# Kernel tuning notes

Hardware: AMD Instinct MI355X
Metric: run time of the kernel (lower is better)

## Reference

```python
import jax, jax.numpy as jnp
import numpy as np

N = 50000      # num nodes
E = 800000     # num edges
D = 128        # num_hid
EPS = 1e-8


def _mlp(x, w1, b1, w2, b2):
    # 2-layer MLP: Linear -> ReLU -> Linear (dropout disabled at inference)
    return jax.nn.relu(x @ w1 + b1) @ w2 + b2


def setup_inputs() -> dict:
    key = jax.random.key(0)
    ks = jax.random.split(key, 12)

    def lin(k, fan_in, fan_out):
        kw, kb = jax.random.split(k)
        lim = 1.0 / np.sqrt(fan_in)
        w = jax.random.uniform(kw, (fan_in, fan_out), jnp.float32, -lim, lim)
        b = jax.random.uniform(kb, (fan_out,), jnp.float32, -lim, lim)
        return w, b

    H = jax.random.normal(ks[0], (N, D), jnp.float32)
    edge_index = jax.random.randint(ks[1], (2, E), 0, N, jnp.int64)
    w1_1, b1_1 = lin(ks[2], 2 * D, D)   # mlp_1 layer 1
    w1_2, b1_2 = lin(ks[3], D, D)       # mlp_1 layer 2
    w2_1, b2_1 = lin(ks[4], 2 * D, D)   # mlp_2 layer 1
    w2_2, b2_2 = lin(ks[5], D, 1)       # mlp_2 layer 2 (channel_curv=False -> out=1)
    t = jnp.zeros((), jnp.float32)
    return {"t": t, "H": H, "edge_index": edge_index,
            "w1_1": w1_1, "b1_1": b1_1, "w1_2": w1_2, "b1_2": b1_2,
            "w2_1": w2_1, "b2_1": b2_1, "w2_2": w2_2, "b2_2": b2_2}


def reference(t, H, edge_index, w1_1, b1_1, w1_2, b1_2, w2_1, b2_1, w2_2, b2_2):
    src, dst = edge_index[0], edge_index[1]

    # damping: row-normalize H
    H = H / (jnp.linalg.norm(H, axis=1, keepdims=True) + EPS)

    H_i = H[src]                                    # [E, D]
    H_j = H[dst]                                    # [E, D]

    # curvature(H_i, H_j)
    c = jnp.concatenate((H_i, H_j), axis=1)         # [E, 2D]
    c = jax.nn.relu(_mlp(c, w1_1, b1_1, w1_2, b1_2))  # [E, D]
    c = jax.ops.segment_sum(c, src, num_segments=N)   # scatter-sum -> [N, D]
    c = jnp.concatenate((c[src], c[dst]), axis=1)     # [E, 2D]
    curv = _mlp(c, w2_1, b2_1, w2_2, b2_2)            # [E, 1]

    # damped edge message
    cos = jnp.sum(H_i * H_j, axis=1, keepdims=True)   # [E, 1]
    H_edge = curv * (H_j - cos * H_i)                 # [E, D]

    # scatter-mean over source node
    s = jax.ops.segment_sum(H_edge, src, num_segments=N)               # [N, D]
    cnt = jax.ops.segment_sum(jnp.ones((E, 1), H.dtype), src, num_segments=N)
    Hm = s / jnp.maximum(cnt, 1.0)

    # damping: row-normalize output
    return Hm / (jnp.linalg.norm(Hm, axis=1, keepdims=True) + EPS)
```

## Files before the change

### kernel.cpp

```cpp
#include <hip/hip_runtime.h>
#include <hip/hip_bf16.h>

#define D 128
#define EPS 1e-8f
#define E1S 136

typedef _Float16 f16;
typedef __attribute__((ext_vector_type(8))) _Float16 half8;
typedef __attribute__((ext_vector_type(4))) float f32x4;
typedef unsigned int uint;

__device__ inline float2 up2(uint u) {
    union { uint u; f16 h[2]; } v; v.u = u;
    return make_float2((float)v.h[0], (float)v.h[1]);
}

__global__ void k_normalize(const float* __restrict__ H, f16* __restrict__ Hn, int N) {
    int row = blockIdx.x * 4 + (threadIdx.x >> 6);
    int lane = threadIdx.x & 63;
    if (row >= N) return;
    float2 v = reinterpret_cast<const float2*>(H + (size_t)row * D)[lane];
    float ss = v.x * v.x + v.y * v.y;
    #pragma unroll
    for (int off = 32; off; off >>= 1) ss += __shfl_xor(ss, off, 64);
    float scale = 1.0f / (sqrtf(ss) + EPS);
    union { f16 h[2]; uint u; } p;
    p.h[0] = (f16)(v.x * scale);
    p.h[1] = (f16)(v.y * scale);
    reinterpret_cast<uint*>(Hn + (size_t)row * D)[lane] = p.u;
}

__global__ void k_hist(const int* __restrict__ src, int* __restrict__ deg, int E) {
    for (int e = blockIdx.x * blockDim.x + threadIdx.x; e < E; e += gridDim.x * blockDim.x)
        atomicAdd(&deg[src[e]], 1);
}

__global__ void k_scan(const int* __restrict__ deg, int* __restrict__ rowptr, int N) {
    __shared__ int wsum[16];
    __shared__ int carry;
    int t = threadIdx.x, lane = t & 63, w = t >> 6;
    if (t == 0) carry = 0;
    __syncthreads();
    for (int base = 0; base < N; base += 4096) {
        int i0 = base + t * 4;
        int a = 0, b = 0, c = 0, d = 0;
        if (i0 + 3 < N) {
            int4 v4 = *reinterpret_cast<const int4*>(deg + i0);
            a = v4.x; b = v4.y; c = v4.z; d = v4.w;
        } else {
            if (i0 < N) a = deg[i0];
            if (i0 + 1 < N) b = deg[i0 + 1];
            if (i0 + 2 < N) c = deg[i0 + 2];
            if (i0 + 3 < N) d = deg[i0 + 3];
        }
        int s1 = a + b, s2 = s1 + c, s3 = s2 + d;
        int v = s3;
        #pragma unroll
        for (int off = 1; off < 64; off <<= 1) {
            int u = __shfl_up(v, off, 64);
            if (lane >= off) v += u;
        }
        if (lane == 63) wsum[w] = v;
        __syncthreads();
        if (w == 0 && lane < 16) {
            int s = wsum[lane];
            #pragma unroll
            for (int off = 1; off < 16; off <<= 1) {
                int u = __shfl_up(s, off, 64);
                if (lane >= off) s += u;
            }
            wsum[lane] = s;
        }
        __syncthreads();
        int add = (w > 0 ? wsum[w - 1] : 0) + carry;
        int incl = v + add;
        int pre = incl - s3;
        if (i0 < N)     rowptr[i0 + 1] = pre + a;
        if (i0 + 1 < N) rowptr[i0 + 2] = pre + s1;
        if (i0 + 2 < N) rowptr[i0 + 3] = pre + s2;
        if (i0 + 3 < N) rowptr[i0 + 4] = pre + s3;
        __syncthreads();
        if (t == 1023) carry = incl;
        __syncthreads();
    }
    if (t == 0) rowptr[0] = 0;
}

__global__ void k_scatter(const int* __restrict__ src, const int* __restrict__ dst,
                          const int* __restrict__ rowptr, int* __restrict__ fill,
                          int* __restrict__ srcS, int* __restrict__ dstS, int E) {
    for (int e = blockIdx.x * blockDim.x + threadIdx.x; e < E; e += gridDim.x * blockDim.x) {
        int s = src[e];
        int pos = atomicAdd(&fill[s], 1);
        int idx = rowptr[s] + pos;
        srcS[idx] = s;
        dstS[idx] = dst[e];
    }
}

__global__ void k_prep_all(const float* __restrict__ w1_1, const float* __restrict__ w1_2,
                           const float* __restrict__ w2_1, f16* __restrict__ Wt) {
    int b = blockIdx.x;
    int m = b >> 6;
    int idx = (b & 63) * 256 + threadIdx.x;
    int k = idx >> 7, n = idx & 127;
    const float* W = (m == 0) ? w1_1
                   : (m == 1) ? w1_1 + 16384
                   : (m == 2) ? w1_2
                   : (m == 3) ? w2_1
                              : w2_1 + 16384;
    Wt[m * 16384 + n * 128 + k] = (f16)W[k * 128 + n];
}

template <bool A_F16>
__global__ __launch_bounds__(256, 4)
void k_gemm_dual(const void* __restrict__ Aptr, const f16* __restrict__ Wt0,
                 const f16* __restrict__ Wt1, const float* __restrict__ bias0,
                 f16* __restrict__ out0, f16* __restrict__ out1, int N) {
    __shared__ f16 As[64 * E1S];
    int t = threadIdx.x;
    int r0 = blockIdx.x * 64;
    int l = t & 63, w = t >> 6, n0 = w * 32;
    {
        int er = t >> 2, kb = (t & 3) * 32;
        int rc = min(r0 + er, N - 1);
        if (A_F16) {
            const half8* Ap = reinterpret_cast<const half8*>((const f16*)Aptr + (size_t)rc * 128 + kb);
            #pragma unroll
            for (int q = 0; q < 4; ++q)
                *reinterpret_cast<half8*>(&As[er * E1S + kb + q * 8]) = Ap[q];
        } else {
            const float4* Ap = reinterpret_cast<const float4*>((const float*)Aptr + (size_t)rc * 128 + kb);
            #pragma unroll
            for (int q = 0; q < 4; ++q) {
                float4 a0 = Ap[q * 2], a1 = Ap[q * 2 + 1];
                half8 sv;
                sv[0] = (f16)a0.x; sv[1] = (f16)a0.y; sv[2] = (f16)a0.z; sv[3] = (f16)a0.w;
                sv[4] = (f16)a1.x; sv[5] = (f16)a1.y; sv[6] = (f16)a1.z; sv[7] = (f16)a1.w;
                *reinterpret_cast<half8*>(&As[er * E1S + kb + q * 8]) = sv;
            }
        }
    }
    half8 bfrag[2][4];
    #pragma unroll
    for (int nt = 0; nt < 2; ++nt) {
        int col = n0 + nt * 16 + (l & 15);
        #pragma unroll
        for (int kt = 0; kt < 4; ++kt)
            bfrag[nt][kt] = *reinterpret_cast<const half8*>(Wt0 + col * 128 + kt * 32 + (l >> 4) * 8);
    }
    float b0a = bias0[n0 + (l & 15)];
    float b0b = bias0[n0 + 16 + (l & 15)];
    __syncthreads();
    f32x4 acc0[4][2], acc1[4][2];
    #pragma unroll
    for (int mt = 0; mt < 4; ++mt) {
        acc0[mt][0] = (f32x4){0,0,0,0}; acc0[mt][1] = (f32x4){0,0,0,0};
        acc1[mt][0] = (f32x4){0,0,0,0}; acc1[mt][1] = (f32x4){0,0,0,0};
    }
    #pragma unroll
    for (int mt = 0; mt < 4; ++mt) {
        int arow = mt * 16 + (l & 15);
        #pragma unroll
        for (int kt = 0; kt < 4; ++kt) {
            half8 af = *reinterpret_cast<const half8*>(&As[arow * E1S + kt * 32 + (l >> 4) * 8]);
            acc0[mt][0] = __builtin_amdgcn_mfma_f32_16x16x32_f16(af, bfrag[0][kt], acc0[mt][0], 0, 0, 0);
            acc0[mt][1] = __builtin_amdgcn_mfma_f32_16x16x32_f16(af, bfrag[1][kt], acc0[mt][1], 0, 0, 0);
        }
    }
    #pragma unroll
    for (int nt = 0; nt < 2; ++nt) {
        int col = n0 + nt * 16 + (l & 15);
        #pragma unroll
        for (int kt = 0; kt < 4; ++kt)
            bfrag[nt][kt] = *reinterpret_cast<const half8*>(Wt1 + col * 128 + kt * 32 + (l >> 4) * 8);
    }
    #pragma unroll
    for (int mt = 0; mt < 4; ++mt) {
        int arow = mt * 16 + (l & 15);
        #pragma unroll
        for (int kt = 0; kt < 4; ++kt) {
            half8 af = *reinterpret_cast<const half8*>(&As[arow * E1S + kt * 32 + (l >> 4) * 8]);
            acc1[mt][0] = __builtin_amdgcn_mfma_f32_16x16x32_f16(af, bfrag[0][kt], acc1[mt][0], 0, 0, 0);
            acc1[mt][1] = __builtin_amdgcn_mfma_f32_16x16x32_f16(af, bfrag[1][kt], acc1[mt][1], 0, 0, 0);
        }
    }
    __syncthreads();
    #pragma unroll
    for (int mt = 0; mt < 4; ++mt)
        #pragma unroll
        for (int j = 0; j < 4; ++j) {
            int row = mt * 16 + (l >> 4) * 4 + j;
            As[row * E1S + n0 + (l & 15)]      = (f16)(acc0[mt][0][j] + b0a);
            As[row * E1S + n0 + 16 + (l & 15)] = (f16)(acc0[mt][1][j] + b0b);
        }
    __syncthreads();
    {
        int er = t >> 2, kb = (t & 3) * 32;
        int row = r0 + er;
        if (row < N)
            #pragma unroll
            for (int q = 0; q < 4; ++q)
                *reinterpret_cast<half8*>(out0 + (size_t)row * 128 + kb + q * 8) =
                    *reinterpret_cast<const half8*>(&As[er * E1S + kb + q * 8]);
    }
    __syncthreads();
    #pragma unroll
    for (int mt = 0; mt < 4; ++mt)
        #pragma unroll
        for (int j = 0; j < 4; ++j) {
            int row = mt * 16 + (l >> 4) * 4 + j;
            As[row * E1S + n0 + (l & 15)]      = (f16)acc1[mt][0][j];
            As[row * E1S + n0 + 16 + (l & 15)] = (f16)acc1[mt][1][j];
        }
    __syncthreads();
    {
        int er = t >> 2, kb = (t & 3) * 32;
        int row = r0 + er;
        if (row < N)
            #pragma unroll
            for (int q = 0; q < 4; ++q)
                *reinterpret_cast<half8*>(out1 + (size_t)row * 128 + kb + q * 8) =
                    *reinterpret_cast<const half8*>(&As[er * E1S + kb + q * 8]);
    }
}

__global__ __launch_bounds__(256, 5)
void k_edge_mlp1(const int* __restrict__ srcS, const int* __restrict__ dstS,
                 const int* __restrict__ rowptr,
                 const f16* __restrict__ P, const f16* __restrict__ Q,
                 const f16* __restrict__ Wt, const float* __restrict__ b1_2,
                 float* __restrict__ C, int E) {
    __shared__ f16 e1s[64 * E1S];
    int t = threadIdx.x;
    int e0 = blockIdx.x * 64;
    int l = t & 63, w = t >> 6, n0 = w * 32;
    {
        int er = t >> 2, kb = (t & 3) * 32;
        int ge = min(e0 + er, E - 1);
        int sc = srcS[ge], dj = dstS[ge];
        const half8* Pp = reinterpret_cast<const half8*>(P + (size_t)sc * 128 + kb);
        const half8* Qp = reinterpret_cast<const half8*>(Q + (size_t)dj * 128 + kb);
        #pragma unroll
        for (int q = 0; q < 4; ++q) {
            half8 sv = Pp[q] + Qp[q];
            #pragma unroll
            for (int i = 0; i < 8; ++i)
                sv[i] = sv[i] > (f16)0 ? sv[i] : (f16)0;
            *reinterpret_cast<half8*>(&e1s[er * E1S + kb + q * 8]) = sv;
        }
    }
    half8 bfrag[2][4];
    #pragma unroll
    for (int nt = 0; nt < 2; ++nt) {
        int col = n0 + nt * 16 + (l & 15);
        #pragma unroll
        for (int kt = 0; kt < 4; ++kt)
            bfrag[nt][kt] = *reinterpret_cast<const half8*>(Wt + col * 128 + kt * 32 + (l >> 4) * 8);
    }
    float bias0 = b1_2[n0 + (l & 15)];
    float bias1 = b1_2[n0 + 16 + (l & 15)];
    __syncthreads();
    f32x4 acc[4][2];
    #pragma unroll
    for (int mt = 0; mt < 4; ++mt) { acc[mt][0] = (f32x4){0,0,0,0}; acc[mt][1] = (f32x4){0,0,0,0}; }
    #pragma unroll
    for (int mt = 0; mt < 4; ++mt) {
        int arow = mt * 16 + (l & 15);
        #pragma unroll
        for (int kt = 0; kt < 4; ++kt) {
            half8 af = *reinterpret_cast<const half8*>(&e1s[arow * E1S + kt * 32 + (l >> 4) * 8]);
            acc[mt][0] = __builtin_amdgcn_mfma_f32_16x16x32_f16(af, bfrag[0][kt], acc[mt][0], 0, 0, 0);
            acc[mt][1] = __builtin_amdgcn_mfma_f32_16x16x32_f16(af, bfrag[1][kt], acc[mt][1], 0, 0, 0);
        }
    }
    #pragma unroll
    for (int mt = 0; mt < 4; ++mt)
        #pragma unroll
        for (int j = 0; j < 4; ++j) {
            acc[mt][0][j] = fmaxf(acc[mt][0][j] + bias0, 0.f);
            acc[mt][1][j] = fmaxf(acc[mt][1][j] + bias1, 0.f);
        }
    int myv = (e0 + l < E) ? srcS[e0 + l] : -1;
    int pv = __shfl_up(myv, 1, 64);
    bool head = (l == 0) || (myv != pv);
    unsigned long long validm = __ballot(myv >= 0);
    unsigned long long hm = __ballot(head) & validm;
    int nvalid = __popcll(validm);
    int grp = l >> 4;
    while (hm) {
        int lo = __builtin_ctzll(hm);
        hm &= hm - 1;
        int hi = hm ? __builtin_ctzll(hm) : nvalid;
        int s = __shfl(myv, lo, 64);
        float v0 = 0.f, v1 = 0.f;
        #pragma unroll
        for (int mt = 0; mt < 4; ++mt)
            #pragma unroll
            for (int j = 0; j < 4; ++j) {
                int row = mt * 16 + grp * 4 + j;
                bool in = (row >= lo) && (row < hi);
                v0 += in ? acc[mt][0][j] : 0.f;
                v1 += in ? acc[mt][1][j] : 0.f;
            }
        v0 += __shfl_xor(v0, 16, 64); v0 += __shfl_xor(v0, 32, 64);
        v1 += __shfl_xor(v1, 16, 64); v1 += __shfl_xor(v1, 32, 64);
        if (l < 16) {
            int rs = rowptr[s], re = rowptr[s + 1];
            float* cp = C + (size_t)s * 128 + n0 + l;
            if (rs >= e0 && re <= e0 + 64) {
                cp[0] = v0; cp[16] = v1;
            } else {
                atomicAdd(cp, v0); atomicAdd(cp + 16, v1);
            }
        }
    }
}

__global__ void k_node_curv(const int* __restrict__ dstS, const int* __restrict__ rowptr,
                            const f16* __restrict__ Hn,
                            const f16* __restrict__ Rb, const f16* __restrict__ Tb,
                            const float* __restrict__ w2_2, const float* __restrict__ b2_2,
                            float* __restrict__ out, int N) {
    int node = blockIdx.x * 4 + (threadIdx.x >> 6);
    int lane = threadIdx.x & 63;
    if (node >= N) return;
    int sub = lane & 15;
    int slot = lane >> 4;
    const uint4* HnU = reinterpret_cast<const uint4*>(Hn);
    const uint4* TbU = reinterpret_cast<const uint4*>(Tb);
    uint4 hiu = HnU[(size_t)node * 16 + sub];
    uint4 rvu = reinterpret_cast<const uint4*>(Rb)[(size_t)node * 16 + sub];
    float hif[8], rvf[8], wvf[8];
    {
        const uint* hp = &hiu.x;
        const uint* rp = &rvu.x;
        float4 w0 = reinterpret_cast<const float4*>(w2_2)[sub * 2];
        float4 w1 = reinterpret_cast<const float4*>(w2_2)[sub * 2 + 1];
        #pragma unroll
        for (int k = 0; k < 4; ++k) {
            float2 h = up2(hp[k]); hif[k * 2] = h.x; hif[k * 2 + 1] = h.y;
            float2 r = up2(rp[k]); rvf[k * 2] = r.x; rvf[k * 2 + 1] = r.y;
        }
        wvf[0] = w0.x; wvf[1] = w0.y; wvf[2] = w0.z; wvf[3] = w0.w;
        wvf[4] = w1.x; wvf[5] = w1.y; wvf[6] = w1.z; wvf[7] = w1.w;
    }
    float bb = b2_2[0];
    int lo = rowptr[node], hiE = rowptr[node + 1];
    int deg = hiE - lo;
    float ax[8];
    #pragma unroll
    for (int j = 0; j < 8; ++j) ax[j] = 0.f;
    float sc = 0.f;
    for (int it = 0; it < deg; it += 4) {
        int e = lo + it + slot;
        bool valid = e < hiE;
        int d = valid ? dstS[e] : 0;
        uint4 hju = HnU[(size_t)d * 16 + sub];
        uint4 tvu = TbU[(size_t)d * 16 + sub];
        float hjf[8];
        float pcos = 0.f, pcur = 0.f;
        {
            const uint* hp = &hju.x;
            const uint* tp = &tvu.x;
            #pragma unroll
            for (int k = 0; k < 4; ++k) {
                float2 h = up2(hp[k]);
                float2 tv = up2(tp[k]);
                hjf[k * 2] = h.x; hjf[k * 2 + 1] = h.y;
                pcos += hif[k * 2] * h.x + hif[k * 2 + 1] * h.y;
                pcur += fmaxf(rvf[k * 2] + tv.x, 0.f) * wvf[k * 2]
                      + fmaxf(rvf[k * 2 + 1] + tv.y, 0.f) * wvf[k * 2 + 1];
            }
        }
        #pragma unroll
        for (int off = 1; off < 16; off <<= 1) {
            pcos += __shfl_xor(pcos, off, 64);
            pcur += __shfl_xor(pcur, off, 64);
        }
        float cur = valid ? (pcur + bb) : 0.f;
        #pragma unroll
        for (int j = 0; j < 8; ++j) ax[j] += cur * hjf[j];
        sc += cur * pcos;
    }
    #pragma unroll
    for (int j = 0; j < 8; ++j) {
        ax[j] += __shfl_xor(ax[j], 16, 64);
        ax[j] += __shfl_xor(ax[j], 32, 64);
    }
    sc += __shfl_xor(sc, 16, 64);
    sc += __shfl_xor(sc, 32, 64);
    float inv = 1.0f / fmaxf((float)deg, 1.0f);
    float ss = 0.f;
    #pragma unroll
    for (int j = 0; j < 8; ++j) {
        ax[j] = (ax[j] - sc * hif[j]) * inv;
        ss += ax[j] * ax[j];
    }
    #pragma unroll
    for (int off = 1; off < 16; off <<= 1) ss += __shfl_xor(ss, off, 64);
    float scale = 1.0f / (sqrtf(ss) + EPS);
    if (slot == 0) {
        float4 o0 = make_float4(ax[0] * scale, ax[1] * scale, ax[2] * scale, ax[3] * scale);
        float4 o1 = make_float4(ax[4] * scale, ax[5] * scale, ax[6] * scale, ax[7] * scale);
        float4* op = reinterpret_cast<float4*>(out + (size_t)node * 128 + sub * 8);
        op[0] = o0;
        op[1] = o1;
    }
}

extern "C" void kernel_launch(void* const* d_in, const int* in_sizes, int n_in,
                              void* d_out, int out_size, void* d_ws, size_t ws_size,
                              hipStream_t stream) {
    const float* H    = (const float*)d_in[1];
    const int*   ei   = (const int*)d_in[2];
    const float* w1_1 = (const float*)d_in[3];
    const float* b1_1 = (const float*)d_in[4];
    const float* w1_2 = (const float*)d_in[5];
    const float* b1_2 = (const float*)d_in[6];
    const float* w2_1 = (const float*)d_in[7];
    const float* b2_1 = (const float*)d_in[8];
    const float* w2_2 = (const float*)d_in[9];
    const float* b2_2 = (const float*)d_in[10];

    int N = in_sizes[1] / D;
    int E = in_sizes[2] / 2;
    const int* src = ei;
    const int* dst = ei + E;

    float* out = (float*)d_out;

    f16* Hnb    = (f16*)d_ws;
    f16* Pb     = Hnb + (size_t)N * D;
    f16* Qb     = Pb + (size_t)N * D;
    float* Cb   = (float*)(Qb + (size_t)N * D);
    f16* Wt     = (f16*)(Cb + (size_t)N * D);
    int* deg    = (int*)(Wt + 5 * 16384);
    int* rowptr = deg + N;
    int* fill   = rowptr + N + 1;
    int* srcS   = fill + N;
    int* dstS   = srcS + E;

    hipMemsetAsync(Cb, 0, (size_t)N * D * sizeof(float), stream);
    hipMemsetAsync(deg, 0, (3 * (size_t)N + 1) * sizeof(int), stream);

    k_normalize<<<(N + 3) / 4, 256, 0, stream>>>(H, Hnb, N);
    k_hist<<<1024, 256, 0, stream>>>(src, deg, E);
    k_scan<<<1, 1024, 0, stream>>>(deg, rowptr, N);
    k_scatter<<<1024, 256, 0, stream>>>(src, dst, rowptr, fill, srcS, dstS, E);
    k_prep_all<<<320, 256, 0, stream>>>(w1_1, w1_2, w2_1, Wt);

    k_gemm_dual<true><<<(N + 63) / 64, 256, 0, stream>>>(Hnb, Wt + 0 * 16384, Wt + 1 * 16384,
                                                         b1_1, Pb, Qb, N);
    k_edge_mlp1<<<(E + 63) / 64, 256, 0, stream>>>(srcS, dstS, rowptr, Pb, Qb,
                                                   Wt + 2 * 16384, b1_2, Cb, E);
    k_gemm_dual<false><<<(N + 63) / 64, 256, 0, stream>>>(Cb, Wt + 3 * 16384, Wt + 4 * 16384,
                                                          b2_1, Pb, Qb, N);
    k_node_curv<<<(N + 3) / 4, 256, 0, stream>>>(dstS, rowptr, Hnb, Pb, Qb, w2_2, b2_2, out, N);
}
```

Measured before the change: 357.8 us.

## Process eight edges per wavefront in node_curv and skip masked tile sums

The node curvature kernel now has each lane own 16 feature columns (8 lanes per edge), so a wavefront handles 8 edges per iteration instead of 4. This halves the loop trip count for typical degrees and shortens the per-edge shuffle reductions, but doubles the register footprint per lane and adds one more cross-slot reduction step. The segment-sum epilogue in the MLP kernel now skips 16-row tiles that lie outside a segment and sums fully covered tiles without per-row masking.

New measurement: 381.7 us. +6.7%, slower.

```diff
diff --git a/kernel.cpp b/kernel.cpp
--- a/kernel.cpp
+++ b/kernel.cpp
@@ -295,14 +295,25 @@
         int s = __shfl(myv, lo, 64);
         float v0 = 0.f, v1 = 0.f;
         #pragma unroll
-        for (int mt = 0; mt < 4; ++mt)
-            #pragma unroll
-            for (int j = 0; j < 4; ++j) {
-                int row = mt * 16 + grp * 4 + j;
-                bool in = (row >= lo) && (row < hi);
-                v0 += in ? acc[mt][0][j] : 0.f;
-                v1 += in ? acc[mt][1][j] : 0.f;
+        for (int mt = 0; mt < 4; ++mt) {
+            int tlo = mt * 16, thi = mt * 16 + 16;
+            if (thi <= lo || tlo >= hi) continue;
+            if (lo <= tlo && hi >= thi) {
+                #pragma unroll
+                for (int j = 0; j < 4; ++j) {
+                    v0 += acc[mt][0][j];
+                    v1 += acc[mt][1][j];
+                }
+            } else {
+                #pragma unroll
+                for (int j = 0; j < 4; ++j) {
+                    int row = tlo + grp * 4 + j;
+                    bool in = (row >= lo) && (row < hi);
+                    v0 += in ? acc[mt][0][j] : 0.f;
+                    v1 += in ? acc[mt][1][j] : 0.f;
+                }
             }
+        }
         v0 += __shfl_xor(v0, 16, 64); v0 += __shfl_xor(v0, 32, 64);
         v1 += __shfl_xor(v1, 16, 64); v1 += __shfl_xor(v1, 32, 64);
         if (l < 16) {
@@ -325,87 +336,105 @@
     int node = blockIdx.x * 4 + (threadIdx.x >> 6);
     int lane = threadIdx.x & 63;
     if (node >= N) return;
-    int sub = lane & 15;
-    int slot = lane >> 4;
+    int sub = lane & 7;
+    int slot = lane >> 3;
     const uint4* HnU = reinterpret_cast<const uint4*>(Hn);
     const uint4* TbU = reinterpret_cast<const uint4*>(Tb);
-    uint4 hiu = HnU[(size_t)node * 16 + sub];
-    uint4 rvu = reinterpret_cast<const uint4*>(Rb)[(size_t)node * 16 + sub];
-    float hif[8], rvf[8], wvf[8];
+    float hif[16], rvf[16], wvf[16];
     {
-        const uint* hp = &hiu.x;
-        const uint* rp = &rvu.x;
-        float4 w0 = reinterpret_cast<const float4*>(w2_2)[sub * 2];
-        float4 w1 = reinterpret_cast<const float4*>(w2_2)[sub * 2 + 1];
+        uint4 h0 = HnU[(size_t)node * 16 + sub * 2];
+        uint4 h1 = HnU[(size_t)node * 16 + sub * 2 + 1];
+        uint4 r0 = reinterpret_cast<const uint4*>(Rb)[(size_t)node * 16 + sub * 2];
+        uint4 r1 = reinterpret_cast<const uint4*>(Rb)[(size_t)node * 16 + sub * 2 + 1];
+        const uint* hp0 = &h0.x; const uint* hp1 = &h1.x;
+        const uint* rp0 = &r0.x; const uint* rp1 = &r1.x;
         #pragma unroll
         for (int k = 0; k < 4; ++k) {
-            float2 h = up2(hp[k]); hif[k * 2] = h.x; hif[k * 2 + 1] = h.y;
-            float2 r = up2(rp[k]); rvf[k * 2] = r.x; rvf[k * 2 + 1] = r.y;
-        }
-        wvf[0] = w0.x; wvf[1] = w0.y; wvf[2] = w0.z; wvf[3] = w0.w;
-        wvf[4] = w1.x; wvf[5] = w1.y; wvf[6] = w1.z; wvf[7] = w1.w;
+            float2 a = up2(hp0[k]); hif[k * 2] = a.x; hif[k * 2 + 1] = a.y;
+            float2 b = up2(hp1[k]); hif[8 + k * 2] = b.x; hif[8 + k * 2 + 1] = b.y;
+            float2 c = up2(rp0[k]); rvf[k * 2] = c.x; rvf[k * 2 + 1] = c.y;
+            float2 d = up2(rp1[k]); rvf[8 + k * 2] = d.x; rvf[8 + k * 2 + 1] = d.y;
+        }
+        #pragma unroll
+        for (int k = 0; k < 4; ++k) {
+            float4 wq = reinterpret_cast<const float4*>(w2_2)[sub * 4 + k];
+            wvf[k * 4 + 0] = wq.x; wvf[k * 4 + 1] = wq.y;
+            wvf[k * 4 + 2] = wq.z; wvf[k * 4 + 3] = wq.w;
+        }
     }
     float bb = b2_2[0];
     int lo = rowptr[node], hiE = rowptr[node + 1];
     int deg = hiE - lo;
-    float ax[8];
-    #pragma unroll
-    for (int j = 0; j < 8; ++j) ax[j] = 0.f;
+    float ax[16];
+    #pragma unroll
+    for (int j = 0; j < 16; ++j) ax[j] = 0.f;
     float sc = 0.f;
-    for (int it = 0; it < deg; it += 4) {
+    for (int it = 0; it < deg; it += 8) {
         int e = lo + it + slot;
         bool valid = e < hiE;
         int d = valid ? dstS[e] : 0;
-        uint4 hju = HnU[(size_t)d * 16 + sub];
-        uint4 tvu = TbU[(size_t)d * 16 + sub];
-        float hjf[8];
+        uint4 hj0 = HnU[(size_t)d * 16 + sub * 2];
+        uint4 hj1 = HnU[(size_t)d * 16 + sub * 2 + 1];
+        uint4 tv0 = TbU[(size_t)d * 16 + sub * 2];
+        uint4 tv1 = TbU[(size_t)d * 16 + sub * 2 + 1];
+        float hjf[16];
         float pcos = 0.f, pcur = 0.f;
         {
-            const uint* hp = &hju.x;
-            const uint* tp = &tvu.x;
+            const uint* hp0 = &hj0.x; const uint* hp1 = &hj1.x;
+            const uint* tp0 = &tv0.x; const uint* tp1 = &tv1.x;
             #pragma unroll
             for (int k = 0; k < 4; ++k) {
-                float2 h = up2(hp[k]);
-                float2 tv = up2(tp[k]);
-                hjf[k * 2] = h.x; hjf[k * 2 + 1] = h.y;
-                pcos += hif[k * 2] * h.x + hif[k * 2 + 1] * h.y;
-                pcur += fmaxf(rvf[k * 2] + tv.x, 0.f) * wvf[k * 2]
-                      + fmaxf(rvf[k * 2 + 1] + tv.y, 0.f) * wvf[k * 2 + 1];
+                float2 a = up2(hp0[k]);
+                float2 b = up2(hp1[k]);
+                hjf[k * 2] = a.x; hjf[k * 2 + 1] = a.y;
+                hjf[8 + k * 2] = b.x; hjf[8 + k * 2 + 1] = b.y;
+                pcos += hif[k * 2] * a.x + hif[k * 2 + 1] * a.y
+                      + hif[8 + k * 2] * b.x + hif[8 + k * 2 + 1] * b.y;
+                float2 c = up2(tp0[k]);
+                float2 d2 = up2(tp1[k]);
+                pcur += fmaxf(rvf[k * 2] + c.x, 0.f) * wvf[k * 2]
+                      + fmaxf(rvf[k * 2 + 1] + c.y, 0.f) * wvf[k * 2 + 1]
+                      + fmaxf(rvf[8 + k * 2] + d2.x, 0.f) * wvf[8 + k * 2]
+                      + fmaxf(rvf[8 + k * 2 + 1] + d2.y, 0.f) * wvf[8 + k * 2 + 1];
             }
         }
         #pragma unroll
-        for (int off = 1; off < 16; off <<= 1) {
+        for (int off = 1; off < 8; off <<= 1) {
             pcos += __shfl_xor(pcos, off, 64);
             pcur += __shfl_xor(pcur, off, 64);
         }
         float cur = valid ? (pcur + bb) : 0.f;
         #pragma unroll
-        for (int j = 0; j < 8; ++j) ax[j] += cur * hjf[j];
+        for (int j = 0; j < 16; ++j) ax[j] += cur * hjf[j];
         sc += cur * pcos;
     }
     #pragma unroll
-    for (int j = 0; j < 8; ++j) {
+    for (int j = 0; j < 16; ++j) {
+        ax[j] += __shfl_xor(ax[j], 8, 64);
         ax[j] += __shfl_xor(ax[j], 16, 64);
         ax[j] += __shfl_xor(ax[j], 32, 64);
     }
+    sc += __shfl_xor(sc, 8, 64);
     sc += __shfl_xor(sc, 16, 64);
     sc += __shfl_xor(sc, 32, 64);
     float inv = 1.0f / fmaxf((float)deg, 1.0f);
     float ss = 0.f;
     #pragma unroll
-    for (int j = 0; j < 8; ++j) {
+    for (int j = 0; j < 16; ++j) {
         ax[j] = (ax[j] - sc * hif[j]) * inv;
         ss += ax[j] * ax[j];
     }
     #pragma unroll
-    for (int off = 1; off < 16; off <<= 1) ss += __shfl_xor(ss, off, 64);
+    for (int off = 1; off < 8; off <<= 1) ss += __shfl_xor(ss, off, 64);
     float scale = 1.0f / (sqrtf(ss) + EPS);
     if (slot == 0) {
-        float4 o0 = make_float4(ax[0] * scale, ax[1] * scale, ax[2] * scale, ax[3] * scale);
-        float4 o1 = make_float4(ax[4] * scale, ax[5] * scale, ax[6] * scale, ax[7] * scale);
-        float4* op = reinterpret_cast<float4*>(out + (size_t)node * 128 + sub * 8);
-        op[0] = o0;
-        op[1] = o1;
+        float* op = out + (size_t)node * 128 + sub * 16;
+        #pragma unroll
+        for (int q = 0; q < 4; ++q) {
+            float4 o = make_float4(ax[q * 4 + 0] * scale, ax[q * 4 + 1] * scale,
+                                   ax[q * 4 + 2] * scale, ax[q * 4 + 3] * scale);
+            reinterpret_cast<float4*>(op)[q] = o;
+        }
     }
 }
 
```
